# Kernel optimization log

Hardware: AMD Instinct MI355X
Metric: run time of the kernel (lower is better)

## Reference

```python
import jax, jax.numpy as jnp
import numpy as np

N, D, E, H = 4096, 256, 131072, 8
HID = 512
GS, K = 4, 3            # grid_size, spline_order
COEF = GS + K           # spline basis count per input feature
GRID = (-1.0 + 0.5 * np.arange(-K, GS + K + 1)).astype(np.float32)  # [GS+2K+1]


def setup_inputs() -> dict:
    key = jax.random.key(0)
    ks = jax.random.split(key, 16)
    rn = lambda i, shape, s=0.05: jax.random.normal(ks[i], shape, jnp.float32) * s
    return {
        "x": rn(0, (N, D), 1.0),
        "edge_index": jax.random.randint(ks[1], (2, E), 0, N),
        # GCN update MLP: Linear(D,HID)+SiLU+Linear(HID,D)
        "gcn_w1": rn(2, (HID, D)), "gcn_b1": jnp.zeros((HID,), jnp.float32),
        "gcn_w2": rn(3, (D, HID)), "gcn_b2": jnp.zeros((D,), jnp.float32),
        # Graphormer attention
        "ln_g": jnp.ones((D,), jnp.float32), "ln_b": jnp.zeros((D,), jnp.float32),
        "w_qkv": rn(4, (3 * D, D)), "b_qkv": jnp.zeros((3 * D,), jnp.float32),
        "w_o": rn(5, (D, D)), "b_o": jnp.zeros((D,), jnp.float32),
        "a_w1": rn(6, (HID, D)), "a_b1": jnp.zeros((HID,), jnp.float32),
        "a_w2": rn(7, (D, HID)), "a_b2": jnp.zeros((D,), jnp.float32),
        # BatchNorms (eval mode, running mean 0 / var 1)
        "bn1_g": jnp.ones((D,), jnp.float32), "bn1_b": jnp.zeros((D,), jnp.float32),
        "bn2_g": jnp.ones((D,), jnp.float32), "bn2_b": jnp.zeros((D,), jnp.float32),
        # KAN: two KANLinear layers D->D
        "kan1_base": rn(8, (D, D)), "kan1_spline": rn(9, (D, D, COEF)),
        "kan1_scaler": jnp.ones((D, D), jnp.float32),
        "kan2_base": rn(10, (D, D)), "kan2_spline": rn(11, (D, D, COEF)),
        "kan2_scaler": jnp.ones((D, D), jnp.float32),
    }


def _mlp2(h, w1, b1, w2, b2):
    return jax.nn.silu(h @ w1.T + b1) @ w2.T + b2


def _bn_eval(h, g, b):
    # eval-mode BatchNorm1d with running_mean=0, running_var=1
    return h * (g / jnp.sqrt(1.0 + 1e-5)) + b


def _layer_norm(h, g, b):
    mu = h.mean(-1, keepdims=True)
    var = ((h - mu) ** 2).mean(-1, keepdims=True)
    return (h - mu) / jnp.sqrt(var + 1e-5) * g + b


def _b_splines(x):
    # x: [n, in] -> [n, in, COEF]; Cox-de Boor recursion on uniform grid
    grid = jnp.asarray(GRID)
    xg = x[..., None]
    bases = ((xg >= grid[:-1]) & (xg < grid[1:])).astype(x.dtype)
    for kk in range(1, K + 1):
        left = (xg - grid[: -(kk + 1)]) / (grid[kk:-1] - grid[: -(kk + 1)])
        right = (grid[kk + 1:] - xg) / (grid[kk + 1:] - grid[1:-kk])
        bases = left * bases[..., :-1] + right * bases[..., 1:]
    return bases


def _kan_linear(x, base_w, spline_w, scaler):
    base = jax.nn.silu(x) @ base_w.T
    bs = _b_splines(x)  # [n, in, COEF]
    spline = jnp.einsum('nic,oic->no', bs, spline_w * scaler[:, :, None])
    return base + spline


def reference(x, edge_index, gcn_w1, gcn_b1, gcn_w2, gcn_b2, ln_g, ln_b,
              w_qkv, b_qkv, w_o, b_o, a_w1, a_b1, a_w2, a_b2,
              bn1_g, bn1_b, bn2_g, bn2_b,
              kan1_base, kan1_spline, kan1_scaler,
              kan2_base, kan2_spline, kan2_scaler):
    n = x.shape[0]
    # ---- GCN branch (add self loops, symmetric normalization, scatter-add) ----
    loops = jnp.arange(n)
    src = jnp.concatenate([edge_index[0], loops])
    dst = jnp.concatenate([edge_index[1], loops])
    w = jnp.ones(src.shape, x.dtype)
    deg = jax.ops.segment_sum(w, src, num_segments=n)
    dis = jnp.where(deg > 0, deg ** -0.5, 0.0)
    norm = dis[src] * w * dis[dst]
    aggr = jax.ops.segment_sum(norm[:, None] * x[src], dst, num_segments=n)
    x_m = _mlp2(aggr, gcn_w1, gcn_b1, gcn_w2, gcn_b2)
    x_m = _bn_eval(x_m, bn1_g, bn1_b) + x  # dropout p=0 / eval -> identity
    # ---- Graphormer attention branch (batch=None -> full NxN self-attn) ----
    xn = _layer_norm(x, ln_g, ln_b)
    qkv = xn @ w_qkv.T + b_qkv
    q, k, v = jnp.split(qkv, 3, axis=-1)
    dh = D // H
    heads = lambda t: t.reshape(n, H, dh).transpose(1, 0, 2)  # [H, n, dh]
    scores = jnp.einsum('hnd,hmd->hnm', heads(q), heads(k)) * (dh ** -0.5)
    attn = jax.nn.softmax(scores, axis=-1)
    o = jnp.einsum('hnm,hmd->hnd', attn, heads(v)).transpose(1, 0, 2).reshape(n, D)
    o = o @ w_o.T + b_o
    x_t = _mlp2(o, a_w1, a_b1, a_w2, a_b2)
    x_t = _bn_eval(x_t, bn2_g, bn2_b) + x
    # ---- KAN head ----
    h = x_t + x_m
    h = _kan_linear(h, kan1_base, kan1_spline, kan1_scaler)
    out = _kan_linear(h, kan2_base, kan2_spline, kan2_scaler)
    return out
```

## Files before the change

### kernel.cpp

```cpp
#include <hip/hip_runtime.h>

typedef unsigned short u16;
typedef __attribute__((ext_vector_type(8))) short bf8;
typedef __attribute__((ext_vector_type(4))) float f32x4;

#define DEVINL __device__ __forceinline__

constexpr int NN = 4096, DD = 256, EE = 131072, HHD = 8, HIDN = 512, COEF_ = 7;

DEVINL u16 f2bf(float f) {
  union { float f; unsigned int i; } c; c.f = f;
  unsigned int u = c.i;
  return (u16)((u + 0x7FFFu + ((u >> 16) & 1u)) >> 16);
}
DEVINL unsigned pk2(float a, float b) {
  return (unsigned)f2bf(a) | ((unsigned)f2bf(b) << 16);
}
DEVINL float siluf(float x) { return x / (1.f + __expf(-x)); }


__global__ void degcnt_k(const int* __restrict__ ei, float* __restrict__ deg,
                         int* __restrict__ cnt) {
  int e = blockIdx.x * 256 + threadIdx.x;
  if (e < EE) {
    atomicAdd(&deg[ei[e]], 1.0f);
    atomicAdd(&cnt[ei[EE + e]], 1);
  }
}

__global__ void dis_k(float* __restrict__ deg) {
  int i = blockIdx.x * 256 + threadIdx.x;
  if (i < NN) deg[i] = rsqrtf(deg[i] + 1.0f);
}

__global__ __launch_bounds__(1024) void scan_k(const int* __restrict__ cnt,
    int* __restrict__ rowptr, int* __restrict__ cursor) {
  __shared__ int sm[1024];
  int t = threadIdx.x;
  int4 c = ((const int4*)cnt)[t];
  int tot = c.x + c.y + c.z + c.w;
  sm[t] = tot;
  __syncthreads();
  for (int off = 1; off < 1024; off <<= 1) {
    int v = (t >= off) ? sm[t - off] : 0;
    __syncthreads();
    sm[t] += v;
    __syncthreads();
  }
  int excl = sm[t] - tot;
  int4 r;
  r.x = excl; r.y = excl + c.x; r.z = r.y + c.y; r.w = r.z + c.z;
  ((int4*)rowptr)[t] = r;
  ((int4*)cursor)[t] = r;
  if (t == 1023) rowptr[4096] = excl + tot;
}

__global__ void fill_k(const int* __restrict__ ei, const float* __restrict__ dis,
    int* __restrict__ cursor, int* __restrict__ esrc, float* __restrict__ ew) {
  int e = blockIdx.x * 256 + threadIdx.x;
  if (e < EE) {
    int s = ei[e], t = ei[EE + e];
    int pos = atomicAdd(&cursor[t], 1);
    esrc[pos] = s;
    ew[pos] = dis[s];
  }
}

__global__ __launch_bounds__(256) void gather_k(const float* __restrict__ x,
    const float* __restrict__ dis, const int* __restrict__ rowptr,
    const int* __restrict__ esrc, const float* __restrict__ ew,
    float* __restrict__ aggr) {
  int node = blockIdx.x * 4 + (threadIdx.x >> 6);
  int lane = threadIdx.x & 63;
  int d0 = lane * 4;
  float dn = dis[node];
  const float4 xv = *(const float4*)(x + (size_t)node * DD + d0);
  float4 acc;
  acc.x = dn * xv.x; acc.y = dn * xv.y; acc.z = dn * xv.z; acc.w = dn * xv.w;
  int beg = rowptr[node], end = rowptr[node + 1];
  for (int base = beg; base < end; base += 64) {
    int idx = base + lane;
    int sv = (idx < end) ? esrc[idx] : 0;
    float wv = (idx < end) ? ew[idx] : 0.f;
    int chunk = min(64, end - base);
    int j = 0;
    for (; j + 2 <= chunk; j += 2) {
      int s0 = __shfl(sv, j), s1 = __shfl(sv, j + 1);
      float w0 = __shfl(wv, j), w1 = __shfl(wv, j + 1);
      const float4 v0 = *(const float4*)(x + (size_t)s0 * DD + d0);
      const float4 v1 = *(const float4*)(x + (size_t)s1 * DD + d0);
      acc.x = fmaf(w0, v0.x, acc.x); acc.y = fmaf(w0, v0.y, acc.y);
      acc.z = fmaf(w0, v0.z, acc.z); acc.w = fmaf(w0, v0.w, acc.w);
      acc.x = fmaf(w1, v1.x, acc.x); acc.y = fmaf(w1, v1.y, acc.y);
      acc.z = fmaf(w1, v1.z, acc.z); acc.w = fmaf(w1, v1.w, acc.w);
    }
    if (j < chunk) {
      int s0 = __shfl(sv, j);
      float w0 = __shfl(wv, j);
      const float4 v0 = *(const float4*)(x + (size_t)s0 * DD + d0);
      acc.x = fmaf(w0, v0.x, acc.x); acc.y = fmaf(w0, v0.y, acc.y);
      acc.z = fmaf(w0, v0.z, acc.z); acc.w = fmaf(w0, v0.w, acc.w);
    }
  }
  float4 outv;
  outv.x = dn * acc.x; outv.y = dn * acc.y; outv.z = dn * acc.z; outv.w = dn * acc.w;
  *(float4*)(aggr + (size_t)node * DD + d0) = outv;
}


#define LSW(r, kb) ((((r) * 128 + ((kb) ^ (((r) & 7) << 4)))) >> 1)

template<bool SILU_A, bool SILU_OUT, bool ACCUM, bool A_BF16, bool W_SCALED>
__global__ __launch_bounds__(256) void mgemm(const void* __restrict__ Aptr,
    const float* __restrict__ W, const float* __restrict__ Wsc,
    const float* __restrict__ bias, float* __restrict__ C, int n, int m, int k)
{
  __shared__ u16 Al[128 * 64];
  __shared__ u16 Wl[64 * 64];
  const int tid = threadIdx.x;
  const int wid = tid >> 6, lane = tid & 63;
  const int wr = wid >> 1, wc = wid & 1;
  const int bn = blockIdx.x * 128, bm = blockIdx.y * 64;
  const int ar = tid >> 1, ak0 = (tid & 1) * 32;
  const int wrr = tid >> 2, wk0 = (tid & 3) * 16;

  f32x4 acc[4][2] = {};

  for (int kt = 0; kt < k; kt += 64) {
    if (A_BF16) {
      const u16* Ap = (const u16*)Aptr + (size_t)(bn + ar) * k + kt + ak0;
#pragma unroll
      for (int c = 0; c < 4; ++c) {
        uint4 w = *(const uint4*)(Ap + 8 * c);
        *(uint4*)&Al[LSW(ar, 2 * ak0 + 16 * c)] = w;
      }
    } else {
      const float* Ap = (const float*)Aptr + (size_t)(bn + ar) * k + kt + ak0;
#pragma unroll
      for (int c = 0; c < 4; ++c) {
        float4 u = *(const float4*)(Ap + 8 * c);
        float4 v = *(const float4*)(Ap + 8 * c + 4);
        if (SILU_A) {
          u.x = siluf(u.x); u.y = siluf(u.y); u.z = siluf(u.z); u.w = siluf(u.w);
          v.x = siluf(v.x); v.y = siluf(v.y); v.z = siluf(v.z); v.w = siluf(v.w);
        }
        uint4 w;
        w.x = pk2(u.x, u.y); w.y = pk2(u.z, u.w);
        w.z = pk2(v.x, v.y); w.w = pk2(v.z, v.w);
        *(uint4*)&Al[LSW(ar, 2 * ak0 + 16 * c)] = w;
      }
    }
    {
      const float* Wp = W + (size_t)(bm + wrr) * k + kt + wk0;
#pragma unroll
      for (int c = 0; c < 2; ++c) {
        float fv[8];
        *(float4*)&fv[0] = *(const float4*)(Wp + 8 * c);
        *(float4*)&fv[4] = *(const float4*)(Wp + 8 * c + 4);
        if (W_SCALED) {
          const float* scrow = Wsc + (size_t)(bm + wrr) * 256;
#pragma unroll
          for (int j = 0; j < 8; ++j) {
            unsigned kidx = (unsigned)(kt + wk0 + 8 * c + j);
            fv[j] *= scrow[(kidx * 9363u) >> 16];
          }
        }
        uint4 w;
        w.x = pk2(fv[0], fv[1]); w.y = pk2(fv[2], fv[3]);
        w.z = pk2(fv[4], fv[5]); w.w = pk2(fv[6], fv[7]);
        *(uint4*)&Wl[LSW(wrr, 2 * wk0 + 16 * c)] = w;
      }
    }
    __syncthreads();
#pragma unroll
    for (int kk = 0; kk < 64; kk += 32) {
      const int kb = (kk + (lane >> 4) * 8) * 2;
      bf8 av[4], bv[2];
#pragma unroll
      for (int fr = 0; fr < 4; ++fr) {
        int r = wr * 64 + fr * 16 + (lane & 15);
        av[fr] = *(const bf8*)&Al[LSW(r, kb)];
      }
#pragma unroll
      for (int fc = 0; fc < 2; ++fc) {
        int r = wc * 32 + fc * 16 + (lane & 15);
        bv[fc] = *(const bf8*)&Wl[LSW(r, kb)];
      }
#pragma unroll
      for (int fr = 0; fr < 4; ++fr)
#pragma unroll
        for (int fc = 0; fc < 2; ++fc)
          acc[fr][fc] = __builtin_amdgcn_mfma_f32_16x16x32_bf16(
              av[fr], bv[fc], acc[fr][fc], 0, 0, 0);
    }
    __syncthreads();
  }
#pragma unroll
  for (int fr = 0; fr < 4; ++fr)
#pragma unroll
    for (int fc = 0; fc < 2; ++fc) {
      int col = bm + wc * 32 + fc * 16 + (lane & 15);
      float bb = bias ? bias[col] : 0.f;
#pragma unroll
      for (int j = 0; j < 4; ++j) {
        int row = bn + wr * 64 + fr * 16 + (lane >> 4) * 4 + j;
        size_t idx = (size_t)row * m + col;
        float v = acc[fr][fc][j] + bb;
        if (ACCUM) v += C[idx];
        if (SILU_OUT) v = siluf(v);
        C[idx] = v;
      }
    }
}


__global__ __launch_bounds__(256) void layernorm_k(const float* __restrict__ x,
    const float* __restrict__ g, const float* __restrict__ b, float* __restrict__ xn) {
  int row = blockIdx.x, t = threadIdx.x;
  float v = x[(size_t)row * DD + t];
  float s = v, sq = v * v;
#pragma unroll
  for (int o = 32; o > 0; o >>= 1) { s += __shfl_down(s, o); sq += __shfl_down(sq, o); }
  __shared__ float rs[4], rq[4];
  int wid = t >> 6, lane = t & 63;
  if (lane == 0) { rs[wid] = s; rq[wid] = sq; }
  __syncthreads();
  float S = rs[0] + rs[1] + rs[2] + rs[3];
  float SQ = rq[0] + rq[1] + rq[2] + rq[3];
  float mu = S * (1.f / 256.f);
  float var = SQ * (1.f / 256.f) - mu * mu;
  float inv = rsqrtf(var + 1e-5f);
  xn[(size_t)row * DD + t] = (v - mu) * inv * g[t] + b[t];
}


__global__ __launch_bounds__(256) void cvtqkv_k(const float* __restrict__ in,
                                                u16* __restrict__ out) {
  int i = blockIdx.x * 256 + threadIdx.x;
  int col = i % 768;
  float v = in[i];
  if (col < 256) v *= 0.25500526764f;
  out[i] = f2bf(v);
}


__global__ __launch_bounds__(256) void flash3(const u16* __restrict__ qkv16,
                                              float* __restrict__ attno) {
  const int h = blockIdx.y, qb = blockIdx.x;
  const int tid = threadIdx.x, wid = tid >> 6;
  const int l15 = tid & 15, hi = (tid >> 4) & 3;
  __shared__ u16 Pf[4][2][64][8];

  const bf8 qf = *(const bf8*)(qkv16 +
      (size_t)(qb * 64 + wid * 16 + l15) * 768 + h * 32 + hi * 8);

  float m = -3.0e38f, l = 0.f;
  f32x4 oa0 = {}, oa1 = {};

  for (int t = 0; t < NN; t += 64) {
    f32x4 sc[4];
    const u16* kbase = qkv16 + (size_t)t * 768 + 256 + h * 32 + hi * 8;
#pragma unroll
    for (int f = 0; f < 4; ++f) {
      bf8 kf = *(const bf8*)(kbase + (size_t)(f * 16 + l15) * 768);
      f32x4 z = {};
      sc[f] = __builtin_amdgcn_mfma_f32_16x16x32_bf16(kf, qf, z, 0, 0, 0);
    }
    bf8 vf[2][2];
    const u16* vbase = qkv16 + (size_t)t * 768 + 512 + h * 32;
#pragma unroll
    for (int s = 0; s < 2; ++s)
#pragma unroll
      for (int a = 0; a < 2; ++a) {
        const u16* vp = vbase + (size_t)(s * 32 + hi * 8) * 768 + a * 16 + l15;
#pragma unroll
        for (int i = 0; i < 8; ++i) vf[s][a][i] = (short)vp[(size_t)i * 768];
      }
    float mx = sc[0][0];
#pragma unroll
    for (int f = 0; f < 4; ++f)
#pragma unroll
      for (int j = 0; j < 4; ++j) mx = fmaxf(mx, sc[f][j]);
    mx = fmaxf(mx, __shfl_xor(mx, 16));
    mx = fmaxf(mx, __shfl_xor(mx, 32));
    float mn = fmaxf(m, mx);
    float scale = exp2f(m - mn);
    m = mn;
    float sum = 0.f;
#pragma unroll
    for (int f = 0; f < 4; ++f)
#pragma unroll
      for (int j = 0; j < 4; ++j) { sc[f][j] = exp2f(sc[f][j] - mn); sum += sc[f][j]; }
    sum += __shfl_xor(sum, 16);
    sum += __shfl_xor(sum, 32);
    l = l * scale + sum;
#pragma unroll
    for (int j = 0; j < 4; ++j) {
      float scj = __shfl(scale, hi * 4 + j);
      oa0[j] *= scj; oa1[j] *= scj;
    }
#pragma unroll
    for (int f = 0; f < 4; ++f) {
      unsigned lo, hi2;
      asm("v_cvt_pk_bf16_f32 %0, %1, %2" : "=v"(lo) : "v"(sc[f][0]), "v"(sc[f][1]));
      asm("v_cvt_pk_bf16_f32 %0, %1, %2" : "=v"(hi2) : "v"(sc[f][2]), "v"(sc[f][3]));
      uint2 pr; pr.x = lo; pr.y = hi2;
      *(uint2*)&Pf[wid][f >> 1][l15 | (((f * 2 + (hi >> 1)) & 3) << 4)][(hi & 1) * 4] = pr;
    }
#pragma unroll
    for (int s = 0; s < 2; ++s) {
      bf8 pa = *(const bf8*)&Pf[wid][s][l15 | (hi << 4)][0];
      oa0 = __builtin_amdgcn_mfma_f32_16x16x32_bf16(pa, vf[s][0], oa0, 0, 0, 0);
      oa1 = __builtin_amdgcn_mfma_f32_16x16x32_bf16(pa, vf[s][1], oa1, 0, 0, 0);
    }
  }
#pragma unroll
  for (int j = 0; j < 4; ++j) {
    float lj = __shfl(l, hi * 4 + j);
    float inv = 1.f / lj;
    int q = qb * 64 + wid * 16 + hi * 4 + j;
    attno[(size_t)q * DD + h * 32 + l15] = oa0[j] * inv;
    attno[(size_t)q * DD + h * 32 + 16 + l15] = oa1[j] * inv;
  }
}


__global__ __launch_bounds__(256) void ew_bn_res_k(float* __restrict__ io,
    const float* __restrict__ g, const float* __restrict__ b,
    const float* __restrict__ x, const float* __restrict__ extra) {
  int i = blockIdx.x * 256 + threadIdx.x;
  int d = i & 255;
  float s = g[d] * rsqrtf(1.0f + 1e-5f);
  float v = io[i] * s + b[d] + x[i];
  if (extra) v += extra[i];
  io[i] = v;
}


__global__ __launch_bounds__(256) void bspl_all_k(const float* __restrict__ h,
                                                  u16* __restrict__ bases) {
  int i = blockIdx.x * 256 + threadIdx.x;
  float v = h[i];
  float b[10];
#pragma unroll
  for (int j = 0; j < 10; ++j) {
    float g0 = 0.5f * j - 2.5f;
    b[j] = (v >= g0 && v < g0 + 0.5f) ? 1.f : 0.f;
  }
#pragma unroll
  for (int kk = 1; kk <= 3; ++kk) {
    float inv = 2.f / (float)kk;
#pragma unroll
    for (int j = 0; j + kk < 10; ++j) {
      float g0 = 0.5f * j - 2.5f;
      float g1 = 0.5f * (j + kk + 1) - 2.5f;
      b[j] = (v - g0) * inv * b[j] + (g1 - v) * inv * b[j + 1];
    }
  }
  u16* o = bases + (size_t)i * 7;
#pragma unroll
  for (int c = 0; c < 7; ++c) o[c] = f2bf(b[c]);
}


extern "C" void kernel_launch(void* const* d_in, const int* in_sizes, int n_in,
                              void* d_out, int out_size, void* d_ws, size_t ws_size,
                              hipStream_t stream) {
  const float* x      = (const float*)d_in[0];
  const int* ei       = (const int*)d_in[1];
  const float* gcn_w1 = (const float*)d_in[2];
  const float* gcn_b1 = (const float*)d_in[3];
  const float* gcn_w2 = (const float*)d_in[4];
  const float* gcn_b2 = (const float*)d_in[5];
  const float* ln_g   = (const float*)d_in[6];
  const float* ln_b   = (const float*)d_in[7];
  const float* w_qkv  = (const float*)d_in[8];
  const float* b_qkv  = (const float*)d_in[9];
  const float* w_o    = (const float*)d_in[10];
  const float* b_o    = (const float*)d_in[11];
  const float* a_w1   = (const float*)d_in[12];
  const float* a_b1   = (const float*)d_in[13];
  const float* a_w2   = (const float*)d_in[14];
  const float* a_b2   = (const float*)d_in[15];
  const float* bn1_g  = (const float*)d_in[16];
  const float* bn1_b  = (const float*)d_in[17];
  const float* bn2_g  = (const float*)d_in[18];
  const float* bn2_b  = (const float*)d_in[19];
  const float* k1_base = (const float*)d_in[20];
  const float* k1_spl  = (const float*)d_in[21];
  const float* k1_scl  = (const float*)d_in[22];
  const float* k2_base = (const float*)d_in[23];
  const float* k2_spl  = (const float*)d_in[24];
  const float* k2_scl  = (const float*)d_in[25];

  float* outF = (float*)d_out;

  const size_t ND = (size_t)NN * DD;
  const size_t BASES_F = 3670016;

  float* ws = (float*)d_ws;
  float* dis    = ws;
  int*   cnt    = (int*)(dis + NN);
  int*   rowptr = cnt + NN;
  int*   cursor = rowptr + NN + 1;
  int*   esrc   = cursor + NN;
  float* ew     = (float*)(esrc + EE);
  float* R1   = ew + EE;
  float* R5   = R1 + ND;
  float* R4   = R5 + (size_t)NN * HIDN;
  float* R2   = R4 + ND;
  float* R3   = R2 + ND;
  float* R6   = R3 + BASES_F;

  float* aggr = R1; float* attno = R1;
  float* mid  = R5; u16* qkv16 = (u16*)R5;
  float* xm   = R4;
  float* xn   = R2; float* h1 = R2;
  float* qkvb = R3; u16* bases = (u16*)R3;
  float* hbuf = R6;

  const dim3 B256(256);

  hipMemsetAsync(dis, 0, NN * (sizeof(float) + sizeof(int)), stream);
  degcnt_k<<<EE / 256, B256, 0, stream>>>(ei, dis, cnt);
  dis_k<<<NN / 256, B256, 0, stream>>>(dis);
  scan_k<<<1, 1024, 0, stream>>>(cnt, rowptr, cursor);
  fill_k<<<EE / 256, B256, 0, stream>>>(ei, dis, cursor, esrc, ew);
  gather_k<<<NN / 4, B256, 0, stream>>>(x, dis, rowptr, esrc, ew, aggr);
  mgemm<false, true, false, false, false><<<dim3(32, HIDN / 64), B256, 0, stream>>>(
      aggr, gcn_w1, nullptr, gcn_b1, mid, NN, HIDN, DD);
  mgemm<false, false, false, false, false><<<dim3(32, DD / 64), B256, 0, stream>>>(
      mid, gcn_w2, nullptr, gcn_b2, xm, NN, DD, HIDN);
  ew_bn_res_k<<<ND / 256, B256, 0, stream>>>(xm, bn1_g, bn1_b, x, nullptr);

  layernorm_k<<<NN, B256, 0, stream>>>(x, ln_g, ln_b, xn);
  mgemm<false, false, false, false, false><<<dim3(32, 768 / 64), B256, 0, stream>>>(
      xn, w_qkv, nullptr, b_qkv, qkvb, NN, 3 * DD, DD);
  cvtqkv_k<<<(NN * 768) / 256, B256, 0, stream>>>(qkvb, qkv16);
  flash3<<<dim3(NN / 64, HHD), B256, 0, stream>>>(qkv16, attno);
  mgemm<false, false, false, false, false><<<dim3(32, DD / 64), B256, 0, stream>>>(
      attno, w_o, nullptr, b_o, xn, NN, DD, DD);
  mgemm<false, true, false, false, false><<<dim3(32, HIDN / 64), B256, 0, stream>>>(
      xn, a_w1, nullptr, a_b1, mid, NN, HIDN, DD);
  mgemm<false, false, false, false, false><<<dim3(32, DD / 64), B256, 0, stream>>>(
      mid, a_w2, nullptr, a_b2, hbuf, NN, DD, HIDN);
  ew_bn_res_k<<<ND / 256, B256, 0, stream>>>(hbuf, bn2_g, bn2_b, x, xm);

  bspl_all_k<<<ND / 256, B256, 0, stream>>>(hbuf, bases);
  mgemm<true, false, false, false, false><<<dim3(32, DD / 64), B256, 0, stream>>>(
      hbuf, k1_base, nullptr, nullptr, h1, NN, DD, DD);
  mgemm<false, false, true, true, true><<<dim3(32, DD / 64), B256, 0, stream>>>(
      bases, k1_spl, k1_scl, nullptr, h1, NN, DD, DD * COEF_);

  bspl_all_k<<<ND / 256, B256, 0, stream>>>(h1, bases);
  mgemm<true, false, false, false, false><<<dim3(32, DD / 64), B256, 0, stream>>>(
      h1, k2_base, nullptr, nullptr, outF, NN, DD, DD);
  mgemm<false, false, true, true, true><<<dim3(32, DD / 64), B256, 0, stream>>>(
      bases, k2_spl, k2_scl, nullptr, outF, NN, DD, DD * COEF_);
}
```

Baseline: 601.1 us.

## Fuse epilogues into GEMMs, prefetch tiles, transpose V, concat KAN base+spline GEMM

Measured after the change: 549.1 us. 1.09x faster.

```diff
diff --git a/kernel.cpp b/kernel.cpp
--- a/kernel.cpp
+++ b/kernel.cpp
@@ -110,112 +110,133 @@
 
 #define LSW(r, kb) ((((r) * 128 + ((kb) ^ (((r) & 7) << 4)))) >> 1)
 
-template<bool SILU_A, bool SILU_OUT, bool ACCUM, bool A_BF16, bool W_SCALED>
-__global__ __launch_bounds__(256) void mgemm(const void* __restrict__ Aptr,
-    const float* __restrict__ W, const float* __restrict__ Wsc,
-    const float* __restrict__ bias, float* __restrict__ C, int n, int m, int k)
+template<int EP, bool A_BF16, bool W_KAN>
+__global__ __launch_bounds__(256) void mgemm(
+    const void* __restrict__ Aptr, const float* __restrict__ Wb,
+    const float* __restrict__ Wspl, const float* __restrict__ Wscl,
+    const float* __restrict__ bias, const float* __restrict__ gam,
+    const float* __restrict__ bet, const float* __restrict__ xres,
+    const float* __restrict__ extra, float* __restrict__ C,
+    u16* __restrict__ q16, u16* __restrict__ Vt, int n, int m, int k)
 {
-  __shared__ u16 Al[128 * 64];
+  __shared__ u16 Al[64 * 64];
   __shared__ u16 Wl[64 * 64];
   const int tid = threadIdx.x;
   const int wid = tid >> 6, lane = tid & 63;
+  const int l15 = lane & 15, hi16 = lane >> 4;
   const int wr = wid >> 1, wc = wid & 1;
-  const int bn = blockIdx.x * 128, bm = blockIdx.y * 64;
-  const int ar = tid >> 1, ak0 = (tid & 1) * 32;
-  const int wrr = tid >> 2, wk0 = (tid & 3) * 16;
-
-  f32x4 acc[4][2] = {};
-
-  for (int kt = 0; kt < k; kt += 64) {
+  const int bn = blockIdx.x * 64, bm = blockIdx.y * 64;
+  const int sr = tid >> 2, sc0 = (tid & 3) * 16;
+
+  float rAf[16];
+  uint4 rAb[2];
+  float rW[16];
+
+  auto loadA = [&](int kt) {
     if (A_BF16) {
-      const u16* Ap = (const u16*)Aptr + (size_t)(bn + ar) * k + kt + ak0;
-#pragma unroll
-      for (int c = 0; c < 4; ++c) {
-        uint4 w = *(const uint4*)(Ap + 8 * c);
-        *(uint4*)&Al[LSW(ar, 2 * ak0 + 16 * c)] = w;
+      const u16* Ap = (const u16*)Aptr + (size_t)(bn + sr) * k + kt + sc0;
+      rAb[0] = *(const uint4*)Ap;
+      rAb[1] = *(const uint4*)(Ap + 8);
+    } else {
+      const float* Ap = (const float*)Aptr + (size_t)(bn + sr) * k + kt + sc0;
+#pragma unroll
+      for (int c = 0; c < 4; ++c) *(float4*)&rAf[c * 4] = *(const float4*)(Ap + c * 4);
+    }
+  };
+  auto loadW = [&](int kt) {
+    if (W_KAN && kt >= 256) {
+      int base = kt - 256 + sc0;
+      const float* sp = Wspl + (size_t)(bm + sr) * 1792 + base;
+      const float* sl = Wscl + (size_t)(bm + sr) * 256;
+#pragma unroll
+      for (int j = 0; j < 16; ++j) {
+        unsigned idx = (unsigned)(base + j);
+        rW[j] = sp[j] * sl[(idx * 9363u) >> 16];
       }
     } else {
-      const float* Ap = (const float*)Aptr + (size_t)(bn + ar) * k + kt + ak0;
-#pragma unroll
-      for (int c = 0; c < 4; ++c) {
-        float4 u = *(const float4*)(Ap + 8 * c);
-        float4 v = *(const float4*)(Ap + 8 * c + 4);
-        if (SILU_A) {
-          u.x = siluf(u.x); u.y = siluf(u.y); u.z = siluf(u.z); u.w = siluf(u.w);
-          v.x = siluf(v.x); v.y = siluf(v.y); v.z = siluf(v.z); v.w = siluf(v.w);
-        }
-        uint4 w;
-        w.x = pk2(u.x, u.y); w.y = pk2(u.z, u.w);
-        w.z = pk2(v.x, v.y); w.w = pk2(v.z, v.w);
-        *(uint4*)&Al[LSW(ar, 2 * ak0 + 16 * c)] = w;
+      const float* Wp = Wb + (size_t)(bm + sr) * (W_KAN ? 256 : k) + kt + sc0;
+#pragma unroll
+      for (int c = 0; c < 4; ++c) *(float4*)&rW[c * 4] = *(const float4*)(Wp + c * 4);
+    }
+  };
+  auto writeLDS = [&]() {
+    if (A_BF16) {
+      *(uint4*)&Al[LSW(sr, 2 * sc0)] = rAb[0];
+      *(uint4*)&Al[LSW(sr, 2 * sc0 + 16)] = rAb[1];
+    } else {
+      uint4 w;
+      w.x = pk2(rAf[0], rAf[1]);  w.y = pk2(rAf[2], rAf[3]);
+      w.z = pk2(rAf[4], rAf[5]);  w.w = pk2(rAf[6], rAf[7]);
+      *(uint4*)&Al[LSW(sr, 2 * sc0)] = w;
+      w.x = pk2(rAf[8], rAf[9]);  w.y = pk2(rAf[10], rAf[11]);
+      w.z = pk2(rAf[12], rAf[13]); w.w = pk2(rAf[14], rAf[15]);
+      *(uint4*)&Al[LSW(sr, 2 * sc0 + 16)] = w;
+    }
+    uint4 w;
+    w.x = pk2(rW[0], rW[1]);  w.y = pk2(rW[2], rW[3]);
+    w.z = pk2(rW[4], rW[5]);  w.w = pk2(rW[6], rW[7]);
+    *(uint4*)&Wl[LSW(sr, 2 * sc0)] = w;
+    w.x = pk2(rW[8], rW[9]);  w.y = pk2(rW[10], rW[11]);
+    w.z = pk2(rW[12], rW[13]); w.w = pk2(rW[14], rW[15]);
+    *(uint4*)&Wl[LSW(sr, 2 * sc0 + 16)] = w;
+  };
+
+  f32x4 acc[2][2] = {};
+  loadA(0); loadW(0);
+  for (int kt = 0; kt < k; kt += 64) {
+    __syncthreads();
+    writeLDS();
+    __syncthreads();
+    if (kt + 64 < k) { loadA(kt + 64); loadW(kt + 64); }
+#pragma unroll
+    for (int kk = 0; kk < 64; kk += 32) {
+      const int kb = (kk + hi16 * 8) * 2;
+      bf8 av[2], bv[2];
+      av[0] = *(const bf8*)&Al[LSW(wr * 32 + l15, kb)];
+      av[1] = *(const bf8*)&Al[LSW(wr * 32 + 16 + l15, kb)];
+      bv[0] = *(const bf8*)&Wl[LSW(wc * 32 + l15, kb)];
+      bv[1] = *(const bf8*)&Wl[LSW(wc * 32 + 16 + l15, kb)];
+      acc[0][0] = __builtin_amdgcn_mfma_f32_16x16x32_bf16(av[0], bv[0], acc[0][0], 0, 0, 0);
+      acc[0][1] = __builtin_amdgcn_mfma_f32_16x16x32_bf16(av[0], bv[1], acc[0][1], 0, 0, 0);
+      acc[1][0] = __builtin_amdgcn_mfma_f32_16x16x32_bf16(av[1], bv[0], acc[1][0], 0, 0, 0);
+      acc[1][1] = __builtin_amdgcn_mfma_f32_16x16x32_bf16(av[1], bv[1], acc[1][1], 0, 0, 0);
+    }
+  }
+#pragma unroll
+  for (int fr = 0; fr < 2; ++fr)
+#pragma unroll
+    for (int fc = 0; fc < 2; ++fc) {
+      int col = bm + wc * 32 + fc * 16 + l15;
+      float bb = bias ? bias[col] : 0.f;
+      float gs = 0.f, bt = 0.f;
+      if (EP == 2) {
+        gs = gam[col] * rsqrtf(1.f + 1e-5f);
+        bt = bet[col];
       }
-    }
-    {
-      const float* Wp = W + (size_t)(bm + wrr) * k + kt + wk0;
-#pragma unroll
-      for (int c = 0; c < 2; ++c) {
-        float fv[8];
-        *(float4*)&fv[0] = *(const float4*)(Wp + 8 * c);
-        *(float4*)&fv[4] = *(const float4*)(Wp + 8 * c + 4);
-        if (W_SCALED) {
-          const float* scrow = Wsc + (size_t)(bm + wrr) * 256;
-#pragma unroll
-          for (int j = 0; j < 8; ++j) {
-            unsigned kidx = (unsigned)(kt + wk0 + 8 * c + j);
-            fv[j] *= scrow[(kidx * 9363u) >> 16];
-          }
-        }
-        uint4 w;
-        w.x = pk2(fv[0], fv[1]); w.y = pk2(fv[2], fv[3]);
-        w.z = pk2(fv[4], fv[5]); w.w = pk2(fv[6], fv[7]);
-        *(uint4*)&Wl[LSW(wrr, 2 * wk0 + 16 * c)] = w;
-      }
-    }
-    __syncthreads();
-#pragma unroll
-    for (int kk = 0; kk < 64; kk += 32) {
-      const int kb = (kk + (lane >> 4) * 8) * 2;
-      bf8 av[4], bv[2];
-#pragma unroll
-      for (int fr = 0; fr < 4; ++fr) {
-        int r = wr * 64 + fr * 16 + (lane & 15);
-        av[fr] = *(const bf8*)&Al[LSW(r, kb)];
-      }
-#pragma unroll
-      for (int fc = 0; fc < 2; ++fc) {
-        int r = wc * 32 + fc * 16 + (lane & 15);
-        bv[fc] = *(const bf8*)&Wl[LSW(r, kb)];
-      }
-#pragma unroll
-      for (int fr = 0; fr < 4; ++fr)
-#pragma unroll
-        for (int fc = 0; fc < 2; ++fc)
-          acc[fr][fc] = __builtin_amdgcn_mfma_f32_16x16x32_bf16(
-              av[fr], bv[fc], acc[fr][fc], 0, 0, 0);
-    }
-    __syncthreads();
-  }
-#pragma unroll
-  for (int fr = 0; fr < 4; ++fr)
-#pragma unroll
-    for (int fc = 0; fc < 2; ++fc) {
-      int col = bm + wc * 32 + fc * 16 + (lane & 15);
-      float bb = bias ? bias[col] : 0.f;
 #pragma unroll
       for (int j = 0; j < 4; ++j) {
-        int row = bn + wr * 64 + fr * 16 + (lane >> 4) * 4 + j;
+        int row = bn + wr * 32 + fr * 16 + hi16 * 4 + j;
         size_t idx = (size_t)row * m + col;
         float v = acc[fr][fc][j] + bb;
-        if (ACCUM) v += C[idx];
-        if (SILU_OUT) v = siluf(v);
-        C[idx] = v;
+        if (EP == 1) v = siluf(v);
+        if (EP == 2) {
+          v = (acc[fr][fc][j] + bb) * gs + bt + xres[idx];
+          if (extra) v += extra[idx];
+        }
+        if (EP == 3) {
+          if (col < 256) q16[(size_t)row * 768 + col] = f2bf(v * 0.25500526764f);
+          else if (col < 512) q16[(size_t)row * 768 + col] = f2bf(v);
+          else Vt[(size_t)(col - 512) * 4096 + row] = f2bf(v);
+        } else {
+          C[idx] = v;
+        }
       }
     }
 }
 
 
-__global__ __launch_bounds__(256) void layernorm_k(const float* __restrict__ x,
-    const float* __restrict__ g, const float* __restrict__ b, float* __restrict__ xn) {
+__global__ __launch_bounds__(256) void layernorm16_k(const float* __restrict__ x,
+    const float* __restrict__ g, const float* __restrict__ b, u16* __restrict__ xn) {
   int row = blockIdx.x, t = threadIdx.x;
   float v = x[(size_t)row * DD + t];
   float s = v, sq = v * v;
@@ -230,21 +251,12 @@
   float mu = S * (1.f / 256.f);
   float var = SQ * (1.f / 256.f) - mu * mu;
   float inv = rsqrtf(var + 1e-5f);
-  xn[(size_t)row * DD + t] = (v - mu) * inv * g[t] + b[t];
-}
-
-
-__global__ __launch_bounds__(256) void cvtqkv_k(const float* __restrict__ in,
-                                                u16* __restrict__ out) {
-  int i = blockIdx.x * 256 + threadIdx.x;
-  int col = i % 768;
-  float v = in[i];
-  if (col < 256) v *= 0.25500526764f;
-  out[i] = f2bf(v);
+  xn[(size_t)row * DD + t] = f2bf((v - mu) * inv * g[t] + b[t]);
 }
 
 
 __global__ __launch_bounds__(256) void flash3(const u16* __restrict__ qkv16,
+                                              const u16* __restrict__ Vt,
                                               float* __restrict__ attno) {
   const int h = blockIdx.y, qb = blockIdx.x;
   const int tid = threadIdx.x, wid = tid >> 6;
@@ -267,15 +279,12 @@
       sc[f] = __builtin_amdgcn_mfma_f32_16x16x32_bf16(kf, qf, z, 0, 0, 0);
     }
     bf8 vf[2][2];
-    const u16* vbase = qkv16 + (size_t)t * 768 + 512 + h * 32;
+    const u16* vtb = Vt + (size_t)(h * 32) * 4096 + t;
 #pragma unroll
     for (int s = 0; s < 2; ++s)
 #pragma unroll
-      for (int a = 0; a < 2; ++a) {
-        const u16* vp = vbase + (size_t)(s * 32 + hi * 8) * 768 + a * 16 + l15;
-#pragma unroll
-        for (int i = 0; i < 8; ++i) vf[s][a][i] = (short)vp[(size_t)i * 768];
-      }
+      for (int a = 0; a < 2; ++a)
+        vf[s][a] = *(const bf8*)(vtb + (size_t)(a * 16 + l15) * 4096 + s * 32 + hi * 8);
     float mx = sc[0][0];
 #pragma unroll
     for (int f = 0; f < 4; ++f)
@@ -325,22 +334,13 @@
 }
 
 
-__global__ __launch_bounds__(256) void ew_bn_res_k(float* __restrict__ io,
-    const float* __restrict__ g, const float* __restrict__ b,
-    const float* __restrict__ x, const float* __restrict__ extra) {
-  int i = blockIdx.x * 256 + threadIdx.x;
-  int d = i & 255;
-  float s = g[d] * rsqrtf(1.0f + 1e-5f);
-  float v = io[i] * s + b[d] + x[i];
-  if (extra) v += extra[i];
-  io[i] = v;
-}
-
-
-__global__ __launch_bounds__(256) void bspl_all_k(const float* __restrict__ h,
-                                                  u16* __restrict__ bases) {
+__global__ __launch_bounds__(256) void bsplcat_k(const float* __restrict__ h,
+                                                 u16* __restrict__ cat) {
   int i = blockIdx.x * 256 + threadIdx.x;
   float v = h[i];
+  int row = i >> 8, col = i & 255;
+  u16* crow = cat + (size_t)row * 2048;
+  crow[col] = f2bf(siluf(v));
   float b[10];
 #pragma unroll
   for (int j = 0; j < 10; ++j) {
@@ -357,7 +357,7 @@
       b[j] = (v - g0) * inv * b[j] + (g1 - v) * inv * b[j + 1];
     }
   }
-  u16* o = bases + (size_t)i * 7;
+  u16* o = crow + 256 + col * 7;
 #pragma unroll
   for (int c = 0; c < 7; ++c) o[c] = f2bf(b[c]);
 }
@@ -396,7 +396,6 @@
   float* outF = (float*)d_out;
 
   const size_t ND = (size_t)NN * DD;
-  const size_t BASES_F = 3670016;
 
   float* ws = (float*)d_ws;
   float* dis    = ws;
@@ -405,56 +404,53 @@
   int*   cursor = rowptr + NN + 1;
   int*   esrc   = cursor + NN;
   float* ew     = (float*)(esrc + EE);
-  float* R1   = ew + EE;
-  float* R5   = R1 + ND;
-  float* R4   = R5 + (size_t)NN * HIDN;
-  float* R2   = R4 + ND;
-  float* R3   = R2 + ND;
-  float* R6   = R3 + BASES_F;
+  float* R1 = ew + EE;
+  float* R5 = R1 + ND;
+  float* R4 = R5 + 2 * ND;
+  float* R2 = R4 + ND;
+  float* R3 = R2 + ND;
+  float* R6 = R3 + 4 * ND;
 
   float* aggr = R1; float* attno = R1;
-  float* mid  = R5; u16* qkv16 = (u16*)R5;
+  float* mid  = R5;
   float* xm   = R4;
-  float* xn   = R2; float* h1 = R2;
-  float* qkvb = R3; u16* bases = (u16*)R3;
+  u16* xn16   = (u16*)R2; float* oproj = R2; float* h1 = R2;
+  u16* qkv16  = (u16*)R3;
+  u16* Vt     = (u16*)R3 + (size_t)NN * 768;
+  u16* cat    = (u16*)R3;
   float* hbuf = R6;
 
   const dim3 B256(256);
-
-  hipMemsetAsync(dis, 0, NN * (sizeof(float) + sizeof(int)), stream);
+  const float* np = nullptr;
+  float* nf = nullptr;
+  u16* nu = nullptr;
+
+  (void)hipMemsetAsync(dis, 0, NN * (sizeof(float) + sizeof(int)), stream);
   degcnt_k<<<EE / 256, B256, 0, stream>>>(ei, dis, cnt);
   dis_k<<<NN / 256, B256, 0, stream>>>(dis);
   scan_k<<<1, 1024, 0, stream>>>(cnt, rowptr, cursor);
   fill_k<<<EE / 256, B256, 0, stream>>>(ei, dis, cursor, esrc, ew);
   gather_k<<<NN / 4, B256, 0, stream>>>(x, dis, rowptr, esrc, ew, aggr);
-  mgemm<false, true, false, false, false><<<dim3(32, HIDN / 64), B256, 0, stream>>>(
-      aggr, gcn_w1, nullptr, gcn_b1, mid, NN, HIDN, DD);
-  mgemm<false, false, false, false, false><<<dim3(32, DD / 64), B256, 0, stream>>>(
-      mid, gcn_w2, nullptr, gcn_b2, xm, NN, DD, HIDN);
-  ew_bn_res_k<<<ND / 256, B256, 0, stream>>>(xm, bn1_g, bn1_b, x, nullptr);
-
-  layernorm_k<<<NN, B256, 0, stream>>>(x, ln_g, ln_b, xn);
-  mgemm<false, false, false, false, false><<<dim3(32, 768 / 64), B256, 0, stream>>>(
-      xn, w_qkv, nullptr, b_qkv, qkvb, NN, 3 * DD, DD);
-  cvtqkv_k<<<(NN * 768) / 256, B256, 0, stream>>>(qkvb, qkv16);
-  flash3<<<dim3(NN / 64, HHD), B256, 0, stream>>>(qkv16, attno);
-  mgemm<false, false, false, false, false><<<dim3(32, DD / 64), B256, 0, stream>>>(
-      attno, w_o, nullptr, b_o, xn, NN, DD, DD);
-  mgemm<false, true, false, false, false><<<dim3(32, HIDN / 64), B256, 0, stream>>>(
-      xn, a_w1, nullptr, a_b1, mid, NN, HIDN, DD);
-  mgemm<false, false, false, false, false><<<dim3(32, DD / 64), B256, 0, stream>>>(
-      mid, a_w2, nullptr, a_b2, hbuf, NN, DD, HIDN);
-  ew_bn_res_k<<<ND / 256, B256, 0, stream>>>(hbuf, bn2_g, bn2_b, x, xm);
-
-  bspl_all_k<<<ND / 256, B256, 0, stream>>>(hbuf, bases);
-  mgemm<true, false, false, false, false><<<dim3(32, DD / 64), B256, 0, stream>>>(
-      hbuf, k1_base, nullptr, nullptr, h1, NN, DD, DD);
-  mgemm<false, false, true, true, true><<<dim3(32, DD / 64), B256, 0, stream>>>(
-      bases, k1_spl, k1_scl, nullptr, h1, NN, DD, DD * COEF_);
-
-  bspl_all_k<<<ND / 256, B256, 0, stream>>>(h1, bases);
-  mgemm<true, false, false, false, false><<<dim3(32, DD / 64), B256, 0, stream>>>(
-      h1, k2_base, nullptr, nullptr, outF, NN, DD, DD);
-  mgemm<false, false, true, true, true><<<dim3(32, DD / 64), B256, 0, stream>>>(
-      bases, k2_spl, k2_scl, nullptr, outF, NN, DD, DD * COEF_);
-}
+  mgemm<1, false, false><<<dim3(64, 8), B256, 0, stream>>>(
+      aggr, gcn_w1, np, np, gcn_b1, np, np, np, np, mid, nu, nu, NN, HIDN, DD);
+  mgemm<2, false, false><<<dim3(64, 4), B256, 0, stream>>>(
+      mid, gcn_w2, np, np, gcn_b2, bn1_g, bn1_b, x, np, xm, nu, nu, NN, DD, HIDN);
+
+  layernorm16_k<<<NN, B256, 0, stream>>>(x, ln_g, ln_b, xn16);
+  mgemm<3, true, false><<<dim3(64, 12), B256, 0, stream>>>(
+      xn16, w_qkv, np, np, b_qkv, np, np, np, np, nf, qkv16, Vt, NN, 768, DD);
+  flash3<<<dim3(NN / 64, HHD), B256, 0, stream>>>(qkv16, Vt, attno);
+  mgemm<0, false, false><<<dim3(64, 4), B256, 0, stream>>>(
+      attno, w_o, np, np, b_o, np, np, np, np, oproj, nu, nu, NN, DD, DD);
+  mgemm<1, false, false><<<dim3(64, 8), B256, 0, stream>>>(
+      oproj, a_w1, np, np, a_b1, np, np, np, np, mid, nu, nu, NN, HIDN, DD);
+  mgemm<2, false, false><<<dim3(64, 4), B256, 0, stream>>>(
+      mid, a_w2, np, np, a_b2, bn2_g, bn2_b, x, xm, hbuf, nu, nu, NN, DD, HIDN);
+
+  bsplcat_k<<<ND / 256, B256, 0, stream>>>(hbuf, cat);
+  mgemm<0, true, true><<<dim3(64, 4), B256, 0, stream>>>(
+      cat, k1_base, k1_spl, k1_scl, np, np, np, np, np, h1, nu, nu, NN, DD, 2048);
+  bsplcat_k<<<ND / 256, B256, 0, stream>>>(h1, cat);
+  mgemm<0, true, true><<<dim3(64, 4), B256, 0, stream>>>(
+      cat, k2_base, k2_spl, k2_scl, np, np, np, np, np, outF, nu, nu, NN, DD, 2048);
+}
```
